# Kernel optimization log

Hardware: AMD Instinct MI355X
Metric: run time of the kernel (lower is better)

## Reference

```python
import jax, jax.numpy as jnp
import numpy as np

N = 500_000
CHANNELS = 256
NUM_GRAPHS = 2048


def setup_inputs() -> dict:
    key = jax.random.key(0)
    k1, k2, k3 = jax.random.split(key, 3)
    features = jax.random.normal(k1, (N, CHANNELS), dtype=jnp.float32)
    batch = jnp.sort(jax.random.randint(k2, (N,), 0, NUM_GRAPHS, dtype=jnp.int64))
    batch = batch.at[-1].set(NUM_GRAPHS - 1)  # pin max so num_segments == NUM_GRAPHS
    W_att = jax.random.normal(k3, (CHANNELS, 1), dtype=jnp.float32) * (1.0 / np.sqrt(CHANNELS))
    b_att = jnp.zeros((1,), dtype=jnp.float32)
    return {"features": features, "batch": batch, "W_att": W_att, "b_att": b_att}


def reference(features, batch, W_att, b_att):
    # attention: Linear(channels, 1) -> Sigmoid, per node  [N, 1]
    weights = jax.nn.sigmoid(features @ W_att + b_att)
    # weighted per-graph sum: equivalent to the python loop over batch ids,
    # fused as a single segment reduction. num_segments = batch.max()+1 = NUM_GRAPHS.
    weighted = features * weights  # [N, C]
    out = jax.ops.segment_sum(weighted, batch, num_segments=NUM_GRAPHS)  # [B, C]
    return out
```

## Files before the change

kernel.cpp:

```cpp
#include <hip/hip_runtime.h>


constexpr int kChannels  = 256;
constexpr int kVecPerRow = kChannels / 4;

typedef float vfloat4 __attribute__((ext_vector_type(4)));

__device__ inline int lower_bound_i32(const int* __restrict__ b, int n, int v) {
    int lo = 0, hi = n;
    while (lo < hi) {
        int mid = (lo + hi) >> 1;
        if (b[mid] < v) lo = mid + 1; else hi = mid;
    }
    return lo;
}

__device__ inline float sigmoidf(float x) { return 1.0f / (1.0f + __expf(-x)); }

__device__ inline float dot4(vfloat4 a, vfloat4 b) {
    return a[0] * b[0] + a[1] * b[1] + a[2] * b[2] + a[3] * b[3];
}

__global__ __launch_bounds__(256, 2)
void hgp_seg_kernel(const float* __restrict__ features,
                    const int*   __restrict__ batch,
                    const float* __restrict__ W_att,
                    const float* __restrict__ b_att,
                    float*       __restrict__ out,
                    int n_nodes) {
    const int g    = blockIdx.x;
    const int wv   = threadIdx.x >> 6;
    const int lane = threadIdx.x & 63;
    const int sub  = lane & 15;
    const int grp  = lane >> 4;

    const int seg_start = lower_bound_i32(batch, n_nodes, g);
    const int seg_end   = lower_bound_i32(batch, n_nodes, g + 1);
    const int seg_len   = seg_end - seg_start;

    const int q   = (seg_len + 3) >> 2;
    const int ws_ = seg_start + wv * q;
    const int we_ = min(ws_ + q, seg_end);

    const vfloat4* __restrict__ frow = reinterpret_cast<const vfloat4*>(features);
    const vfloat4* __restrict__ W4   = reinterpret_cast<const vfloat4*>(W_att);

    const vfloat4 w0 = W4[sub];
    const vfloat4 w1 = W4[sub + 16];
    const vfloat4 w2 = W4[sub + 32];
    const vfloat4 w3 = W4[sub + 48];
    const float bias = b_att[0];

    vfloat4 a0 = 0.f, a1 = 0.f, a2 = 0.f, a3 = 0.f;

    int n = ws_;
    vfloat4 c0, c1, c2, c3;

    if (n + 4 <= we_) {
        const size_t rb = (size_t)(n + grp) * kVecPerRow + sub;
        c0 = __builtin_nontemporal_load(&frow[rb]);
        c1 = __builtin_nontemporal_load(&frow[rb + 16]);
        c2 = __builtin_nontemporal_load(&frow[rb + 32]);
        c3 = __builtin_nontemporal_load(&frow[rb + 48]);
    }

    for (; n + 8 <= we_; n += 4) {
        const size_t rb = (size_t)(n + 4 + grp) * kVecPerRow + sub;
        vfloat4 x0 = __builtin_nontemporal_load(&frow[rb]);
        vfloat4 x1 = __builtin_nontemporal_load(&frow[rb + 16]);
        vfloat4 x2 = __builtin_nontemporal_load(&frow[rb + 32]);
        vfloat4 x3 = __builtin_nontemporal_load(&frow[rb + 48]);

        float p = dot4(c0, w0) + dot4(c1, w1) + dot4(c2, w2) + dot4(c3, w3);
        p += __shfl_xor(p, 8, 64);
        p += __shfl_xor(p, 4, 64);
        p += __shfl_xor(p, 2, 64);
        p += __shfl_xor(p, 1, 64);
        const float gate = sigmoidf(p + bias);

        a0 += c0 * gate; a1 += c1 * gate; a2 += c2 * gate; a3 += c3 * gate;

        c0 = x0; c1 = x1; c2 = x2; c3 = x3;
    }

    if (n + 4 <= we_) {
        float p = dot4(c0, w0) + dot4(c1, w1) + dot4(c2, w2) + dot4(c3, w3);
        p += __shfl_xor(p, 8, 64);
        p += __shfl_xor(p, 4, 64);
        p += __shfl_xor(p, 2, 64);
        p += __shfl_xor(p, 1, 64);
        const float gate = sigmoidf(p + bias);
        a0 += c0 * gate; a1 += c1 * gate; a2 += c2 * gate; a3 += c3 * gate;
        n += 4;
    }

    if (n < we_) {
        const int  row = n + grp;
        const bool ok  = row < we_;
        const size_t rb = (size_t)(ok ? row : we_ - 1) * kVecPerRow + sub;
        vfloat4 t0 = __builtin_nontemporal_load(&frow[rb]);
        vfloat4 t1 = __builtin_nontemporal_load(&frow[rb + 16]);
        vfloat4 t2 = __builtin_nontemporal_load(&frow[rb + 32]);
        vfloat4 t3 = __builtin_nontemporal_load(&frow[rb + 48]);
        if (!ok) { t0 = 0.f; t1 = 0.f; t2 = 0.f; t3 = 0.f; }

        float p = dot4(t0, w0) + dot4(t1, w1) + dot4(t2, w2) + dot4(t3, w3);
        p += __shfl_xor(p, 8, 64);
        p += __shfl_xor(p, 4, 64);
        p += __shfl_xor(p, 2, 64);
        p += __shfl_xor(p, 1, 64);
        const float gate = sigmoidf(p + bias);
        a0 += t0 * gate; a1 += t1 * gate; a2 += t2 * gate; a3 += t3 * gate;
    }

    __shared__ float lds[16][kChannels];
    {
        const int slot = wv * 4 + grp;
        vfloat4* dst = reinterpret_cast<vfloat4*>(lds[slot]);
        dst[sub]      = a0;
        dst[sub + 16] = a1;
        dst[sub + 32] = a2;
        dst[sub + 48] = a3;
    }
    __syncthreads();

    const int t = threadIdx.x;
    float s = 0.f;
    #pragma unroll
    for (int k = 0; k < 16; ++k) s += lds[k][t];
    out[(size_t)g * kChannels + t] = s;
}

extern "C" void kernel_launch(void* const* d_in, const int* in_sizes, int n_in,
                              void* d_out, int out_size, void* d_ws, size_t ws_size,
                              hipStream_t stream) {
    const float* features = (const float*)d_in[0];
    const int*   batch    = (const int*)d_in[1];
    const float* W_att    = (const float*)d_in[2];
    const float* b_att    = (const float*)d_in[3];
    float*       out      = (float*)d_out;

    const int n_nodes    = in_sizes[1];
    const int num_graphs = out_size / kChannels;

    hgp_seg_kernel<<<num_graphs, 256, 0, stream>>>(features, batch, W_att, b_att,
                                                   out, n_nodes);
}
```

Measured before the change: 626.6 us.

## Precompute segment offsets in a pre-pass and deepen load prefetch to two stages

Adds a small kernel that turns the sorted batch array into per-graph offsets in workspace memory, so each block reads two ints instead of doing two binary searches over the batch array. The main loop now keeps two row-groups of features in flight instead of one, giving more memory-level parallelism per wave. The cost is one extra kernel launch and more live vector registers, which could lower occupancy under the launch bounds.

```diff
diff --git a/kernel.cpp b/kernel.cpp
--- a/kernel.cpp
+++ b/kernel.cpp
@@ -6,36 +6,39 @@
 
 typedef float vfloat4 __attribute__((ext_vector_type(4)));
 
-__device__ inline int lower_bound_i32(const int* __restrict__ b, int n, int v) {
-    int lo = 0, hi = n;
-    while (lo < hi) {
-        int mid = (lo + hi) >> 1;
-        if (b[mid] < v) lo = mid + 1; else hi = mid;
-    }
-    return lo;
-}
-
 __device__ inline float sigmoidf(float x) { return 1.0f / (1.0f + __expf(-x)); }
 
 __device__ inline float dot4(vfloat4 a, vfloat4 b) {
     return a[0] * b[0] + a[1] * b[1] + a[2] * b[2] + a[3] * b[3];
 }
 
+__global__ void seg_bounds_kernel(const int* __restrict__ batch,
+                                  int* __restrict__ offs,
+                                  int n_nodes, int num_graphs) {
+    const int i = blockIdx.x * blockDim.x + threadIdx.x;
+    if (i >= n_nodes) return;
+    const int b    = batch[i];
+    const int prev = (i == 0) ? -1 : batch[i - 1];
+    for (int v = prev + 1; v <= b; ++v) offs[v] = i;
+    if (i == n_nodes - 1) {
+        for (int v = b + 1; v <= num_graphs; ++v) offs[v] = n_nodes;
+    }
+}
+
 __global__ __launch_bounds__(256, 2)
 void hgp_seg_kernel(const float* __restrict__ features,
-                    const int*   __restrict__ batch,
+                    const int*   __restrict__ offs,
                     const float* __restrict__ W_att,
                     const float* __restrict__ b_att,
-                    float*       __restrict__ out,
-                    int n_nodes) {
+                    float*       __restrict__ out) {
     const int g    = blockIdx.x;
     const int wv   = threadIdx.x >> 6;
     const int lane = threadIdx.x & 63;
     const int sub  = lane & 15;
     const int grp  = lane >> 4;
 
-    const int seg_start = lower_bound_i32(batch, n_nodes, g);
-    const int seg_end   = lower_bound_i32(batch, n_nodes, g + 1);
+    const int seg_start = offs[g];
+    const int seg_end   = offs[g + 1];
     const int seg_len   = seg_end - seg_start;
 
     const int q   = (seg_len + 3) >> 2;
@@ -51,46 +54,59 @@
     const vfloat4 w3 = W4[sub + 48];
     const float bias = b_att[0];
 
-    vfloat4 a0 = 0.f, a1 = 0.f, a2 = 0.f, a3 = 0.f;
+    vfloat4 acc0 = 0.f, acc1 = 0.f, acc2 = 0.f, acc3 = 0.f;
 
     int n = ws_;
-    vfloat4 c0, c1, c2, c3;
+    vfloat4 a0, a1, a2, a3;
+    vfloat4 b0, b1, b2, b3;
 
     if (n + 4 <= we_) {
         const size_t rb = (size_t)(n + grp) * kVecPerRow + sub;
-        c0 = __builtin_nontemporal_load(&frow[rb]);
-        c1 = __builtin_nontemporal_load(&frow[rb + 16]);
-        c2 = __builtin_nontemporal_load(&frow[rb + 32]);
-        c3 = __builtin_nontemporal_load(&frow[rb + 48]);
+        a0 = __builtin_nontemporal_load(&frow[rb]);
+        a1 = __builtin_nontemporal_load(&frow[rb + 16]);
+        a2 = __builtin_nontemporal_load(&frow[rb + 32]);
+        a3 = __builtin_nontemporal_load(&frow[rb + 48]);
+    }
+    if (n + 8 <= we_) {
+        const size_t rb = (size_t)(n + 4 + grp) * kVecPerRow + sub;
+        b0 = __builtin_nontemporal_load(&frow[rb]);
+        b1 = __builtin_nontemporal_load(&frow[rb + 16]);
+        b2 = __builtin_nontemporal_load(&frow[rb + 32]);
+        b3 = __builtin_nontemporal_load(&frow[rb + 48]);
     }
 
-    for (; n + 8 <= we_; n += 4) {
-        const size_t rb = (size_t)(n + 4 + grp) * kVecPerRow + sub;
-        vfloat4 x0 = __builtin_nontemporal_load(&frow[rb]);
-        vfloat4 x1 = __builtin_nontemporal_load(&frow[rb + 16]);
-        vfloat4 x2 = __builtin_nontemporal_load(&frow[rb + 32]);
-        vfloat4 x3 = __builtin_nontemporal_load(&frow[rb + 48]);
+    #define HGP_COMPUTE(r0, r1, r2, r3)                                        \
+        do {                                                                   \
+            float p = dot4(r0, w0) + dot4(r1, w1) + dot4(r2, w2) + dot4(r3, w3); \
+            p += __shfl_xor(p, 8, 64);                                         \
+            p += __shfl_xor(p, 4, 64);                                         \
+            p += __shfl_xor(p, 2, 64);                                         \
+            p += __shfl_xor(p, 1, 64);                                         \
+            const float gate = sigmoidf(p + bias);                             \
+            acc0 += r0 * gate; acc1 += r1 * gate;                              \
+            acc2 += r2 * gate; acc3 += r3 * gate;                              \
+        } while (0)
 
-        float p = dot4(c0, w0) + dot4(c1, w1) + dot4(c2, w2) + dot4(c3, w3);
-        p += __shfl_xor(p, 8, 64);
-        p += __shfl_xor(p, 4, 64);
-        p += __shfl_xor(p, 2, 64);
-        p += __shfl_xor(p, 1, 64);
-        const float gate = sigmoidf(p + bias);
+    for (; n + 12 <= we_; n += 4) {
+        const size_t rb = (size_t)(n + 8 + grp) * kVecPerRow + sub;
+        vfloat4 c0 = __builtin_nontemporal_load(&frow[rb]);
+        vfloat4 c1 = __builtin_nontemporal_load(&frow[rb + 16]);
+        vfloat4 c2 = __builtin_nontemporal_load(&frow[rb + 32]);
+        vfloat4 c3 = __builtin_nontemporal_load(&frow[rb + 48]);
 
-        a0 += c0 * gate; a1 += c1 * gate; a2 += c2 * gate; a3 += c3 * gate;
+        HGP_COMPUTE(a0, a1, a2, a3);
 
-        c0 = x0; c1 = x1; c2 = x2; c3 = x3;
+        a0 = b0; a1 = b1; a2 = b2; a3 = b3;
+        b0 = c0; b1 = c1; b2 = c2; b3 = c3;
     }
 
     if (n + 4 <= we_) {
-        float p = dot4(c0, w0) + dot4(c1, w1) + dot4(c2, w2) + dot4(c3, w3);
-        p += __shfl_xor(p, 8, 64);
-        p += __shfl_xor(p, 4, 64);
-        p += __shfl_xor(p, 2, 64);
-        p += __shfl_xor(p, 1, 64);
-        const float gate = sigmoidf(p + bias);
-        a0 += c0 * gate; a1 += c1 * gate; a2 += c2 * gate; a3 += c3 * gate;
+        HGP_COMPUTE(a0, a1, a2, a3);
+        n += 4;
+        a0 = b0; a1 = b1; a2 = b2; a3 = b3;
+    }
+    if (n + 4 <= we_) {
+        HGP_COMPUTE(a0, a1, a2, a3);
         n += 4;
     }
 
@@ -103,24 +119,18 @@
         vfloat4 t2 = __builtin_nontemporal_load(&frow[rb + 32]);
         vfloat4 t3 = __builtin_nontemporal_load(&frow[rb + 48]);
         if (!ok) { t0 = 0.f; t1 = 0.f; t2 = 0.f; t3 = 0.f; }
-
-        float p = dot4(t0, w0) + dot4(t1, w1) + dot4(t2, w2) + dot4(t3, w3);
-        p += __shfl_xor(p, 8, 64);
-        p += __shfl_xor(p, 4, 64);
-        p += __shfl_xor(p, 2, 64);
-        p += __shfl_xor(p, 1, 64);
-        const float gate = sigmoidf(p + bias);
-        a0 += t0 * gate; a1 += t1 * gate; a2 += t2 * gate; a3 += t3 * gate;
+        HGP_COMPUTE(t0, t1, t2, t3);
     }
+    #undef HGP_COMPUTE
 
     __shared__ float lds[16][kChannels];
     {
         const int slot = wv * 4 + grp;
         vfloat4* dst = reinterpret_cast<vfloat4*>(lds[slot]);
-        dst[sub]      = a0;
-        dst[sub + 16] = a1;
-        dst[sub + 32] = a2;
-        dst[sub + 48] = a3;
+        dst[sub]      = acc0;
+        dst[sub + 16] = acc1;
+        dst[sub + 32] = acc2;
+        dst[sub + 48] = acc3;
     }
     __syncthreads();
 
@@ -139,10 +149,13 @@
     const float* W_att    = (const float*)d_in[2];
     const float* b_att    = (const float*)d_in[3];
     float*       out      = (float*)d_out;
+    int*         offs     = (int*)d_ws;
 
     const int n_nodes    = in_sizes[1];
     const int num_graphs = out_size / kChannels;
 
-    hgp_seg_kernel<<<num_graphs, 256, 0, stream>>>(features, batch, W_att, b_att,
-                                                   out, n_nodes);
+    const int b1 = (n_nodes + 255) / 256;
+    seg_bounds_kernel<<<b1, 256, 0, stream>>>(batch, offs, n_nodes, num_graphs);
+
+    hgp_seg_kernel<<<num_graphs, 256, 0, stream>>>(features, offs, W_att, b_att, out);
 }
```

After: 619.9 us. No clear change (-1.1%).
